# Kernel tuning notes

Measured on AMD Instinct MI355X. Metric: run time of the kernel, lower is better.

## Reference

```python
import jax, jax.numpy as jnp
import numpy as np

N = 9
DIM = 2 ** N  # 512
RANGES = [1, 2, 3]  # PennyLane StronglyEntanglingLayers default: (l % (N-1)) + 1


def _cnot_mat(c, t):
    # CNOT on (control c, target t); wire 0 = most significant bit (default.qubit)
    idx = np.arange(DIM)
    bit = (idx >> (N - 1 - c)) & 1
    new = idx ^ (bit << (N - 1 - t))
    m = np.zeros((DIM, DIM), np.complex64)
    m[new, idx] = 1.0
    return m


def _layer_cnot_ring(r):
    # product of CNOT(i, (i+r) % N) applied for i = 0..N-1 (in circuit order)
    m = np.eye(DIM, dtype=np.complex64)
    for i in range(N):
        m = _cnot_mat(i, (i + r) % N) @ m
    return jnp.asarray(m)


_CNOT_LAYERS = [_layer_cnot_ring(r) for r in RANGES]

# PauliZ diagonal per wire: zd[w, k] = +1/-1 depending on bit w of basis index k
_ZDIAG = jnp.asarray(
    1.0 - 2.0 * (((np.arange(DIM)[None, :] >> (N - 1 - np.arange(N)[:, None])) & 1)),
    dtype=jnp.float32,
)


def _rot2x2(phi, theta, omega):
    # PennyLane Rot = RZ(omega) RY(theta) RZ(phi)
    phi = phi.astype(jnp.complex64)
    theta = theta.astype(jnp.complex64)
    omega = omega.astype(jnp.complex64)
    c = jnp.cos(theta / 2)
    s = jnp.sin(theta / 2)
    m00 = jnp.exp(-0.5j * (phi + omega)) * c
    m01 = -jnp.exp(0.5j * (phi - omega)) * s
    m10 = jnp.exp(-0.5j * (phi - omega)) * s
    m11 = jnp.exp(0.5j * (phi + omega)) * c
    return jnp.stack([jnp.stack([m00, m01]), jnp.stack([m10, m11])])


def _circuit_unitary(weights):
    # Full 512x512 unitary for the 3 StronglyEntanglingLayers (weight-dependent part)
    u = jnp.eye(DIM, dtype=jnp.complex64)
    for l in range(weights.shape[0]):
        rot = _rot2x2(weights[l, 0, 0], weights[l, 0, 1], weights[l, 0, 2])
        for w in range(1, N):
            rot = jnp.kron(rot, _rot2x2(weights[l, w, 0], weights[l, w, 1], weights[l, w, 2]))
        u = _CNOT_LAYERS[l] @ (rot @ u)
    return u


def _forward(x, weights):
    b = x.shape[0]
    # AngleEmbedding (RX) on |0>: per-qubit state [cos(t/2), -i sin(t/2)]
    half = x.astype(jnp.float32) / 2
    q = jnp.stack(
        [jnp.cos(half).astype(jnp.complex64), (-1j) * jnp.sin(half).astype(jnp.complex64)],
        axis=-1,
    )  # [B, 9, 2]
    s = q[:, 0, :]
    for w in range(1, N):  # batched kron across qubits -> [B, 512]
        s = (s[:, :, None] * q[:, w, None, :]).reshape(b, -1)
    u = _circuit_unitary(weights)
    psi = s @ u.T  # [B, 512]
    probs = psi.real ** 2 + psi.imag ** 2  # [B, 512] float32
    return probs @ _ZDIAG.T  # [B, 9] <Z_w> expectations


def setup_inputs() -> dict:
    key = jax.random.key(0)
    k1, k2 = jax.random.split(key)
    return {
        "x": jax.random.normal(k1, (32768, 9), dtype=jnp.float32),
        "weights": jax.random.normal(k2, (3, 9, 3), dtype=jnp.float32),
    }


def reference(x, weights):
    return _forward(x, weights).astype(jnp.float32)
```

## Files before the change

kernel.cpp:

```cpp
#include <hip/hip_runtime.h>
#include <hip/hip_fp16.h>


typedef float v2f __attribute__((ext_vector_type(2)));

constexpr int pf(int l, int i) {
    const int r = l + 1; int j = i;
    for (int c = 0; c < 9; ++c) {
        const int bit = (j >> (8 - c)) & 1;
        const int t = (c + r) % 9;
        j ^= bit << (8 - t);
    }
    return j;
}
constexpr int sg(int i) { return i ^ (i >> 4); }

struct PMask { int m[2][9]; };
constexpr PMask make_pmask() {
    PMask pm{};
    for (int bd = 0; bd < 2; ++bd)
        for (int q = 0; q < 9; ++q) {
            const int img = pf(bd, 1 << q);
            for (int p = 0; p < 9; ++p)
                if ((img >> p) & 1) pm.m[bd][p] |= 1 << q;
        }
    return pm;
}
constexpr PMask PM = make_pmask();

struct T3Tab { int laneBase[2][6]; int regPart[2][8]; };
constexpr T3Tab make_t3() {
    T3Tab t{};
    for (int l = 0; l < 2; ++l) {
        for (int b = 0; b < 6; ++b) t.laneBase[l][b] = sg(pf(l, 1 << b));
        for (int g = 0; g < 8; ++g) t.regPart [l][g] = sg(pf(l, g << 6));
    }
    return t;
}
constexpr T3Tab T3T = make_t3();

constexpr int sgk3(int k) { return (k << 3) ^ (k >> 1); }
constexpr int sgk6(int k) { return (k << 6) ^ (k << 2); }

#define PI_F    3.14159265358979323846f
#define INV2PI  0.15915494309189535f

static __device__ inline unsigned pack_rn(float x, float y) {
    const __half2 h = __floats2half2_rn(x, y);
    return *(const unsigned*)&h;
}

__global__ __launch_bounds__(512) void qtab_kernel(
        const float* __restrict__ wt, float* __restrict__ ws) {
    const int j = threadIdx.x;
    unsigned* wu = (unsigned*)ws;
    if (j < 27) {
        float s, c; __sincosf(0.5f * wt[j * 3 + 1], &s, &c);
        wu[j] = pack_rn(c, s);
    }
    #pragma unroll
    for (int bd = 0; bd < 2; ++bd) {
        float alpha = 0.0f;
        #pragma unroll
        for (int p = 0; p < 9; ++p) {
            const int w = 8 - p;
            const float om = wt[(bd * 9 + w) * 3 + 2];
            const float ph = wt[((bd + 1) * 9 + w) * 3 + 0];
            alpha += ((j >> p) & 1) ? 0.5f * om : -0.5f * om;
            alpha += (__popc(j & PM.m[bd][p]) & 1) ? 0.5f * ph : -0.5f * ph;
        }
        float sn, cs; __sincosf(alpha, &sn, &cs);
        wu[64 + bd * 512 + j] = pack_rn(cs, sn);
    }
    {
        float a = 0.0f;
        #pragma unroll
        for (int p = 0; p < 9; ++p) {
            const int w = 8 - p;
            const float phi = wt[w * 3 + 0];
            a += ((j >> p) & 1) ? (0.5f * phi - 0.5f * PI_F) : (-0.5f * phi);
        }
        float sn, cs; __sincosf(a, &sn, &cs);
        ((v2f*)(ws + 1088))[j] = (v2f){cs, sn};
    }
}

#define APPLY_GATE(G, KB)                                                     \
    {                                                                         \
        _Pragma("unroll")                                                     \
        for (int k0 = 0; k0 < 8; ++k0) if (!(k0 & (KB))) {                    \
            const int k1 = k0 | (KB);                                         \
            unsigned t;                                                       \
            asm("v_pk_mul_f16 %0, %1, %2 op_sel:[0,1] op_sel_hi:[1,1] "       \
                "neg_lo:[0,1] neg_hi:[0,1]"                                   \
                : "=v"(t) : "v"(a[k1]), "s"(G));               \
            asm("v_pk_mul_f16 %0, %0, %1 op_sel:[0,0] op_sel_hi:[1,0]"        \
                : "+v"(a[k1]) : "s"(G));                       \
            asm("v_pk_fma_f16 %0, %1, %2, %0 op_sel:[0,1,0] op_sel_hi:[1,1,1]"\
                : "+v"(a[k1]) : "v"(a[k0]), "s"(G));          \
            asm("v_pk_fma_f16 %0, %0, %1, %2 op_sel:[0,0,0] op_sel_hi:[1,0,1]"\
                : "+v"(a[k0]) : "s"(G), "v"(t));             \
        }                                                                     \
    }

__global__ __launch_bounds__(256) void qsim_kernel(
        const float* __restrict__ x,
        const float* __restrict__ tab,
        float* __restrict__ out,
        int batch) {
    __shared__ unsigned st[4][512];

    const int tid  = threadIdx.x;
    const int wv   = tid >> 6;
    const int lane = tid & 63;
    const int b    = blockIdx.x * 4 + wv;
    if (b >= batch) return;
    const int bu   = __builtin_amdgcn_readfirstlane(b);

    unsigned* __restrict__ S = st[wv];
    const unsigned* __restrict__ tu = (const unsigned*)tab;
    const unsigned* __restrict__ D0 = tu + 64;
    const unsigned* __restrict__ D1 = tu + 576;
    const v2f*     __restrict__ PH = (const v2f*)(tab + 1088);

    float cx[9], sx[9];
    #pragma unroll
    for (int w = 0; w < 9; ++w) {
        const float rev = x[bu * 9 + w] * (0.5f * INV2PI);
        sx[w] = __builtin_amdgcn_sinf(rev);
        cx[w] = __builtin_amdgcn_cosf(rev);
    }
    float P = 1.0f;
    #pragma unroll
    for (int w = 0; w < 6; ++w)
        P *= ((lane >> (5 - w)) & 1) ? sx[w] : cx[w];

    unsigned a[8];
    #pragma unroll
    for (int k = 0; k < 8; ++k) {
        const float m = P * ((k & 4) ? sx[6] : cx[6])
                          * ((k & 2) ? sx[7] : cx[7])
                          * ((k & 1) ? sx[8] : cx[8]);
        const v2f ph = PH[(lane << 3) | k];
        a[k] = pack_rn(ph.x * m, ph.y * m);
    }

    const int baseA = (lane << 3) ^ (lane >> 1);
    const int hB    = ((lane & 0x38) << 3) | (lane & 7);
    const int baseB = hB ^ (hB >> 4);
    const int baseC = lane ^ (lane >> 4);
    int t3b[2];
    #pragma unroll
    for (int l = 0; l < 2; ++l) {
        int v = 0;
        #pragma unroll
        for (int bb = 0; bb < 6; ++bb)
            v ^= ((lane >> bb) & 1) ? T3T.laneBase[l][bb] : 0;
        t3b[l] = v;
    }

    #pragma unroll
    for (int l = 0; l < 3; ++l) {
        unsigned g[9];
        #pragma unroll
        for (int q = 0; q < 9; ++q) g[q] = tu[l * 9 + q];

        APPLY_GATE(g[6], 4);
        APPLY_GATE(g[7], 2);
        APPLY_GATE(g[8], 1);

        #pragma unroll
        for (int k = 0; k < 8; ++k) S[baseA ^ k] = a[k];
        #pragma unroll
        for (int k = 0; k < 8; ++k) a[k] = S[baseB ^ sgk3(k)];

        APPLY_GATE(g[3], 4);
        APPLY_GATE(g[4], 2);
        APPLY_GATE(g[5], 1);

        #pragma unroll
        for (int k = 0; k < 8; ++k) S[baseB ^ sgk3(k)] = a[k];
        #pragma unroll
        for (int k = 0; k < 8; ++k) a[k] = S[baseC ^ sgk6(k)];

        APPLY_GATE(g[0], 4);
        APPLY_GATE(g[1], 2);
        APPLY_GATE(g[2], 1);

        if (l < 2) {
            const unsigned* __restrict__ D = (l == 0) ? D0 : D1;
            #pragma unroll
            for (int k = 0; k < 8; ++k) {
                const unsigned d = D[(k << 6) | lane];
                unsigned t;
                asm("v_pk_mul_f16 %0, %1, %2 op_sel:[1,1] op_sel_hi:[0,1] "
                    "neg_lo:[0,1]"
                    : "=v"(t) : "v"(a[k]), "v"(d));
                asm("v_pk_fma_f16 %0, %1, %2, %3 op_sel:[0,0,0] op_sel_hi:[1,0,1]"
                    : "=v"(a[k]) : "v"(a[k]), "v"(d), "v"(t));
            }
            #pragma unroll
            for (int k = 0; k < 8; ++k)
                S[t3b[l] ^ T3T.regPart[l][k]] = a[k];
            #pragma unroll
            for (int k = 0; k < 8; ++k) a[k] = S[baseA ^ k];
        }
    }

    float A0 = 0.f, A1 = 0.f, A2 = 0.f, A3 = 0.f;
    #pragma unroll
    for (int k = 0; k < 8; ++k) {
        const __half2 h = *(const __half2*)&a[k];
        const float2 f = __half22float2(h);
        const float p = f.x * f.x + f.y * f.y;
        A0 += p;
        A1 += (k & 4) ? -p : p;
        A2 += (k & 2) ? -p : p;
        A3 += (k & 1) ? -p : p;
    }
    v2f F01 = (v2f){A0, A1};
    v2f F23 = (v2f){A2, A3};

    #pragma unroll
    for (int d = 1; d < 64; d <<= 1) {
        const float sg1 = (lane & d) ? -1.0f : 1.0f;
        const v2f sgn = (v2f){sg1, sg1};
        v2f p01, p23;
        p01.x = __shfl_xor(F01.x, d, 64);  p01.y = __shfl_xor(F01.y, d, 64);
        p23.x = __shfl_xor(F23.x, d, 64);  p23.y = __shfl_xor(F23.y, d, 64);
        F01 = F01 * sgn + p01;
        F23 = F23 * sgn + p23;
    }
    float* Sf = (float*)S;
    Sf[2 * lane]           = F01.x;
    Sf[2 * lane + 1]       = F01.y;
    Sf[128 + 2 * lane]     = F23.x;
    Sf[128 + 2 * lane + 1] = F23.y;
    if (lane < 9) {
        const int idx = (lane == 0) ? 72  : (lane == 1) ? 36  : (lane == 2) ? 18
                      : (lane == 3) ? 65  : (lane == 4) ? 160 : (lane == 5) ? 145
                      : (lane == 6) ? 73  : (lane == 7) ? 164 : 147;
        out[bu * 9 + lane] = Sf[idx];
    }
}

extern "C" void kernel_launch(void* const* d_in, const int* in_sizes, int n_in,
                              void* d_out, int out_size, void* d_ws, size_t ws_size,
                              hipStream_t stream) {
    const float* x  = (const float*)d_in[0];
    const float* wt = (const float*)d_in[1];
    float* out = (float*)d_out;
    const int batch = in_sizes[0] / 9;
    float* ws = (float*)d_ws;

    hipLaunchKernelGGL(qtab_kernel, dim3(1), dim3(512), 0, stream, wt, ws);
    hipLaunchKernelGGL(qsim_kernel, dim3((batch + 3) / 4), dim3(256), 0, stream,
                       x, ws, out, batch);
}
```

Before: 103.3 us.

## Redesign LDS transpose layout for 128-bit reads and use fdot2 reductions

Replaces the XOR-swizzled shared-memory layout with a padded-free layout chosen at compile time by searching qubit-bit permutations that bound bank conflicts, so every transpose read becomes two 128-bit LDS loads instead of eight 32-bit loads. Initial amplitude construction now loads phases as float4 and shares partial products across registers. The final probability accumulation uses packed f16 dot-product instructions instead of converting to float. This aims to cut LDS instruction count and ALU work, at the cost of possible write-side bank conflicts and a constexpr search that may fall back to a poor mapping.

```diff
diff --git a/kernel.cpp b/kernel.cpp
--- a/kernel.cpp
+++ b/kernel.cpp
@@ -3,6 +3,7 @@
 
 
 typedef float v2f __attribute__((ext_vector_type(2)));
+typedef _Float16 v2h __attribute__((ext_vector_type(2)));
 
 constexpr int pf(int l, int i) {
     const int r = l + 1; int j = i;
@@ -13,7 +14,6 @@
     }
     return j;
 }
-constexpr int sg(int i) { return i ^ (i >> 4); }
 
 struct PMask { int m[2][9]; };
 constexpr PMask make_pmask() {
@@ -28,19 +28,59 @@
 }
 constexpr PMask PM = make_pmask();
 
-struct T3Tab { int laneBase[2][6]; int regPart[2][8]; };
-constexpr T3Tab make_t3() {
-    T3Tab t{};
-    for (int l = 0; l < 2; ++l) {
-        for (int b = 0; b < 6; ++b) t.laneBase[l][b] = sg(pf(l, 1 << b));
-        for (int g = 0; g < 8; ++g) t.regPart [l][g] = sg(pf(l, g << 6));
-    }
-    return t;
-}
-constexpr T3Tab T3T = make_t3();
-
-constexpr int sgk3(int k) { return (k << 3) ^ (k >> 1); }
-constexpr int sgk6(int k) { return (k << 6) ^ (k << 2); }
+struct Sig3 {
+    int wbasis[6];
+    int koff[8];
+    int rimg[6];
+};
+constexpr Sig3 make_sig3(int l) {
+    Sig3 out{};
+    for (int limit = 2; limit <= 64; limit *= 2) {
+        for (int idx = 0; idx < 720; ++idx) {
+            int pool[6] = {3, 4, 5, 6, 7, 8};
+            int perm[6] = {};
+            int f = idx;
+            const int fact[6] = {120, 24, 6, 2, 1, 1};
+            int n = 6;
+            for (int pos = 0; pos < 6; ++pos) {
+                const int sel = f / fact[pos]; f %= fact[pos];
+                perm[pos] = pool[sel];
+                for (int m2 = sel; m2 + 1 < n; ++m2) pool[m2] = pool[m2 + 1];
+                --n;
+            }
+            int img[9] = {0, 1, 2, perm[0], perm[1], perm[2],
+                          perm[3], perm[4], perm[5]};
+            int cnt[32] = {};
+            bool ok = true;
+            for (int L = 0; L < 64 && ok; ++L) {
+                const int j = pf(l, L);
+                int addr = 0;
+                for (int bb = 0; bb < 9; ++bb)
+                    if ((j >> bb) & 1) addr ^= 1 << img[bb];
+                if (++cnt[addr & 31] > limit) ok = false;
+            }
+            if (ok) {
+                for (int b2 = 0; b2 < 6; ++b2) {
+                    const int j = pf(l, 1 << b2); int v = 0;
+                    for (int bb = 0; bb < 9; ++bb)
+                        if ((j >> bb) & 1) v ^= 1 << img[bb];
+                    out.wbasis[b2] = v;
+                }
+                for (int k = 0; k < 8; ++k) {
+                    const int j = pf(l, k << 6); int v = 0;
+                    for (int bb = 0; bb < 9; ++bb)
+                        if ((j >> bb) & 1) v ^= 1 << img[bb];
+                    out.koff[k] = v;
+                }
+                for (int b2 = 0; b2 < 6; ++b2) out.rimg[b2] = img[3 + b2];
+                return out;
+            }
+        }
+    }
+    return out;
+}
+constexpr Sig3 S3_0 = make_sig3(0);
+constexpr Sig3 S3_1 = make_sig3(1);
 
 #define PI_F    3.14159265358979323846f
 #define INV2PI  0.15915494309189535f
@@ -108,7 +148,7 @@
         const float* __restrict__ tab,
         float* __restrict__ out,
         int batch) {
-    __shared__ unsigned st[4][512];
+    __shared__ uint4 st4[4][128];
 
     const int tid  = threadIdx.x;
     const int wv   = tid >> 6;
@@ -117,11 +157,12 @@
     if (b >= batch) return;
     const int bu   = __builtin_amdgcn_readfirstlane(b);
 
-    unsigned* __restrict__ S = st[wv];
+    unsigned* __restrict__ S  = (unsigned*)st4[wv];
+    const uint4* __restrict__ S4 = st4[wv];
     const unsigned* __restrict__ tu = (const unsigned*)tab;
     const unsigned* __restrict__ D0 = tu + 64;
     const unsigned* __restrict__ D1 = tu + 576;
-    const v2f*     __restrict__ PH = (const v2f*)(tab + 1088);
+    const float4*  __restrict__ PH4 = (const float4*)(tab + 1088);
 
     float cx[9], sx[9];
     #pragma unroll
@@ -135,28 +176,39 @@
     for (int w = 0; w < 6; ++w)
         P *= ((lane >> (5 - w)) & 1) ? sx[w] : cx[w];
 
+    float mk[8];
+    {
+        const float m0 = P * cx[6],  m1 = P * sx[6];
+        const float m00 = m0 * cx[7], m01 = m0 * sx[7];
+        const float m10 = m1 * cx[7], m11 = m1 * sx[7];
+        mk[0] = m00 * cx[8]; mk[1] = m00 * sx[8];
+        mk[2] = m01 * cx[8]; mk[3] = m01 * sx[8];
+        mk[4] = m10 * cx[8]; mk[5] = m10 * sx[8];
+        mk[6] = m11 * cx[8]; mk[7] = m11 * sx[8];
+    }
     unsigned a[8];
     #pragma unroll
-    for (int k = 0; k < 8; ++k) {
-        const float m = P * ((k & 4) ? sx[6] : cx[6])
-                          * ((k & 2) ? sx[7] : cx[7])
-                          * ((k & 1) ? sx[8] : cx[8]);
-        const v2f ph = PH[(lane << 3) | k];
-        a[k] = pack_rn(ph.x * m, ph.y * m);
-    }
-
-    const int baseA = (lane << 3) ^ (lane >> 1);
-    const int hB    = ((lane & 0x38) << 3) | (lane & 7);
-    const int baseB = hB ^ (hB >> 4);
-    const int baseC = lane ^ (lane >> 4);
-    int t3b[2];
+    for (int j2 = 0; j2 < 4; ++j2) {
+        const float4 ph = PH4[(lane << 2) + j2];
+        a[2 * j2]     = pack_rn(ph.x * mk[2 * j2],     ph.y * mk[2 * j2]);
+        a[2 * j2 + 1] = pack_rn(ph.z * mk[2 * j2 + 1], ph.w * mk[2 * j2 + 1]);
+    }
+
+    const int wb1 = (lane & 31) | ((lane & 32) << 3);
+    const int rb1 = ((lane & 7) << 5) | (lane & 0x18) | ((lane & 32) << 3);
+    const int wb2 = ((lane >> 3) & 7) | ((lane & 3) << 3) | ((lane & 4) << 6);
+    const int rb2 = ((lane & 3) << 3) | ((lane & 4) << 6) | ((lane & 0x38) << 2);
+    int t3b[2], rb3[2];
     #pragma unroll
     for (int l = 0; l < 2; ++l) {
-        int v = 0;
-        #pragma unroll
-        for (int bb = 0; bb < 6; ++bb)
-            v ^= ((lane >> bb) & 1) ? T3T.laneBase[l][bb] : 0;
-        t3b[l] = v;
+        int tb = 0, rb = 0;
+        #pragma unroll
+        for (int bb = 0; bb < 6; ++bb) {
+            const int on = (lane >> bb) & 1;
+            tb ^= on ? (l ? S3_1.wbasis[bb] : S3_0.wbasis[bb]) : 0;
+            rb ^= on ? (1 << (l ? S3_1.rimg[bb] : S3_0.rimg[bb])) : 0;
+        }
+        t3b[l] = tb; rb3[l] = rb;
     }
 
     #pragma unroll
@@ -170,18 +222,26 @@
         APPLY_GATE(g[8], 1);
 
         #pragma unroll
-        for (int k = 0; k < 8; ++k) S[baseA ^ k] = a[k];
-        #pragma unroll
-        for (int k = 0; k < 8; ++k) a[k] = S[baseB ^ sgk3(k)];
+        for (int k = 0; k < 8; ++k) S[wb1 + (k << 5)] = a[k];
+        {
+            const uint4 r0 = S4[(rb1 >> 2)];
+            const uint4 r1 = S4[(rb1 >> 2) + 1];
+            a[0] = r0.x; a[1] = r0.y; a[2] = r0.z; a[3] = r0.w;
+            a[4] = r1.x; a[5] = r1.y; a[6] = r1.z; a[7] = r1.w;
+        }
 
         APPLY_GATE(g[3], 4);
         APPLY_GATE(g[4], 2);
         APPLY_GATE(g[5], 1);
 
         #pragma unroll
-        for (int k = 0; k < 8; ++k) S[baseB ^ sgk3(k)] = a[k];
-        #pragma unroll
-        for (int k = 0; k < 8; ++k) a[k] = S[baseC ^ sgk6(k)];
+        for (int k = 0; k < 8; ++k) S[wb2 + (k << 5)] = a[k];
+        {
+            const uint4 r0 = S4[(rb2 >> 2)];
+            const uint4 r1 = S4[(rb2 >> 2) + 1];
+            a[0] = r0.x; a[1] = r0.y; a[2] = r0.z; a[3] = r0.w;
+            a[4] = r1.x; a[5] = r1.y; a[6] = r1.z; a[7] = r1.w;
+        }
 
         APPLY_GATE(g[0], 4);
         APPLY_GATE(g[1], 2);
@@ -201,15 +261,28 @@
             }
             #pragma unroll
             for (int k = 0; k < 8; ++k)
-                S[t3b[l] ^ T3T.regPart[l][k]] = a[k];
-            #pragma unroll
-            for (int k = 0; k < 8; ++k) a[k] = S[baseA ^ k];
+                S[t3b[l] ^ (l ? S3_1.koff[k] : S3_0.koff[k])] = a[k];
+            {
+                const uint4 r0 = S4[(rb3[l] >> 2)];
+                const uint4 r1 = S4[(rb3[l] >> 2) + 1];
+                a[0] = r0.x; a[1] = r0.y; a[2] = r0.z; a[3] = r0.w;
+                a[4] = r1.x; a[5] = r1.y; a[6] = r1.z; a[7] = r1.w;
+            }
         }
     }
 
     float A0 = 0.f, A1 = 0.f, A2 = 0.f, A3 = 0.f;
     #pragma unroll
     for (int k = 0; k < 8; ++k) {
+#if __has_builtin(__builtin_amdgcn_fdot2)
+        v2h h, hn;
+        { unsigned u = a[k];               h = *(const v2h*)&u; }
+        { unsigned un = a[k] ^ 0x80008000u; hn = *(const v2h*)&un; }
+        A0 = __builtin_amdgcn_fdot2(h, h, A0, false);
+        A1 = __builtin_amdgcn_fdot2(h, (k & 4) ? hn : h, A1, false);
+        A2 = __builtin_amdgcn_fdot2(h, (k & 2) ? hn : h, A2, false);
+        A3 = __builtin_amdgcn_fdot2(h, (k & 1) ? hn : h, A3, false);
+#else
         const __half2 h = *(const __half2*)&a[k];
         const float2 f = __half22float2(h);
         const float p = f.x * f.x + f.y * f.y;
@@ -217,6 +290,7 @@
         A1 += (k & 4) ? -p : p;
         A2 += (k & 2) ? -p : p;
         A3 += (k & 1) ? -p : p;
+#endif
     }
     v2f F01 = (v2f){A0, A1};
     v2f F23 = (v2f){A2, A3};
```

Result: faster. 99.27 us (-3.9%).
